# Kernel tuning notes

Hardware: AMD Instinct MI355X
Metric: run time of the kernel (lower is better)

Reference implementation:

```python
import jax, jax.numpy as jnp
import numpy as np

DIM = 256
NUM_RFS = 256
OUT_DIM = 1024
N = 65536
M = 0.001


def setup_inputs() -> dict:
    key = jax.random.key(0)
    k1, k2, k3, k4, k5, k6 = jax.random.split(key, 6)
    x = jax.random.normal(k1, (N, DIM), dtype=jnp.float32)
    input_weights = jax.random.normal(k2, (OUT_DIM, DIM), dtype=jnp.float32)
    b = jax.random.normal(k3, (OUT_DIM,), dtype=jnp.float32)
    # projection matrix: normal(mean=0, std=0.02, size=(num_rfs, dim))
    proj = 0.02 * jax.random.normal(k4, (NUM_RFS, DIM), dtype=jnp.float32)
    # xis are complex points of the random-feature construction; keep small for exp stability
    xis_real = 0.1 * jax.random.normal(k5, (NUM_RFS,), dtype=jnp.float32)
    xis_imag = 0.1 * jax.random.normal(k6, (NUM_RFS,), dtype=jnp.float32)
    return {"x": x, "input_weights": input_weights, "b": b, "proj": proj,
            "xis_real": xis_real, "xis_imag": xis_imag}


def _asym_feats(xw, xis, proj, bias, is_weight):
    """create_asym_feats with a_fun/b_fun = identity, A_fun/B_fun = exp(xi*b).
    xw: (rows, DIM) float; xis: (NUM_RFS,) complex64; proj: (NUM_RFS, DIM) float.
    Returns (rows, NUM_RFS) complex64."""
    ab = xis  # ab_fun is identity -> ab_coeffs = xis
    scale = np.sqrt(1.0 + 4.0 * M).astype(np.float32)
    # renorm_gs[i] = sqrt(1+4M) * ab[i] * gs[i]  -> (NUM_RFS, DIM) complex
    renorm_gs = scale * ab[:, None] * proj.astype(jnp.complex64)
    # dot_products = xw_c @ renorm_gs.T  -> (rows, NUM_RFS) complex
    dot = jnp.einsum('nd,rd->nr', xw.astype(jnp.complex64), renorm_gs)
    sq = jnp.sum(xw * xw, axis=-1)  # (rows,)
    # correction: outer(sq/2, ab*ab) + M*||g_i||^2 (broadcast over rows)
    corr = (sq[:, None] * 0.5) * (ab * ab)[None, :]
    corr = corr + M * jnp.sum(proj * proj, axis=-1)[None, :]
    feats = jnp.exp(dot - corr) * np.float32(1.0 / np.sqrt(NUM_RFS))
    if is_weight:
        # AB_coeffs[j, i] = exp(xis[i] * bias[j])
        AB = jnp.exp(xis[None, :] * bias[:, None].astype(jnp.complex64))
        feats = AB * feats
    return feats


def reference(x, input_weights, b, proj, xis_real, xis_imag):
    xis = (xis_real + 1j * xis_imag).astype(jnp.complex64)
    # normalize=False path: scale weights and bias by dim**-0.25 at init time
    inv4 = np.float32(1.0 / DIM ** 0.25)
    w = input_weights * inv4
    bb = b * inv4
    c = np.float32((1.0 / np.sqrt(2.0)) * (1.0 + 4.0 * M) ** (DIM / 4.0))
    # precomputed weight features (parameter of the module)
    w_plus = _asym_feats(w, xis, proj, bb, is_weight=True)
    w_minus = _asym_feats(w, -xis, proj, bb, is_weight=True)
    weights = c * jnp.concatenate([w_plus, w_minus], axis=-1)  # (OUT_DIM, 2R) complex
    # forward: x scaled by 1/dim (normalize=False)
    xs = x * np.float32(1.0 / DIM)
    f_plus = _asym_feats(xs, xis, proj, bb, is_weight=False)
    f_minus = _asym_feats(xs, -xis, proj, bb, is_weight=False)
    feat = c * jnp.concatenate([f_plus, f_minus], axis=-1)  # (N, 2R) complex
    # (feat @ weights.T).real
    out = jnp.einsum('nr,or->no', feat, weights).real
    return out
```

## Files before the change

### kernel.cpp

```cpp
#include <hip/hip_runtime.h>
#include <cmath>
#include <cstdint>

#define NROWS 65536
#define DIMN  256
#define NRF   256
#define OUTD  1024
#define KDIM  1024
#define MCOEF 0.001f

typedef __bf16 v8bf __attribute__((ext_vector_type(8)));
typedef float  v4f  __attribute__((ext_vector_type(4)));
typedef unsigned short us8 __attribute__((ext_vector_type(8)));

__device__ __forceinline__ unsigned short f2bf(float f) {
  unsigned int u = __float_as_uint(f);
  u += 0x7fffu + ((u >> 16) & 1u);
  return (unsigned short)(u >> 16);
}

__device__ __forceinline__ void async_copy16(const void* g, void* l) {
  __builtin_amdgcn_global_load_lds(
      (const __attribute__((address_space(1))) void*)g,
      (__attribute__((address_space(3))) void*)l, 16, 0, 0);
}

__device__ __forceinline__ int sw_slot(int r, int c) {
  return r * 4 + ((c ^ (r >> 1)) & 3);
}

__global__ __launch_bounds__(64) void prep_rf(
    const float* __restrict__ proj, unsigned short* __restrict__ projbf,
    float* __restrict__ mg2) {
  int i = blockIdx.x;
  int lane = threadIdx.x;
  float4 v = ((const float4*)(proj + (size_t)i * DIMN))[lane];
  ushort4 o;
  o.x = f2bf(v.x); o.y = f2bf(v.y); o.z = f2bf(v.z); o.w = f2bf(v.w);
  ((ushort4*)(projbf + (size_t)i * DIMN))[lane] = o;
  float ss = v.x * v.x + v.y * v.y + v.z * v.z + v.w * v.w;
#pragma unroll
  for (int off = 32; off > 0; off >>= 1) ss += __shfl_down(ss, off, 64);
  if (lane == 0) mg2[i] = MCOEF * ss;
}

__global__ __launch_bounds__(256) void fused_features(
    const float* __restrict__ src,
    float scl,
    const float* __restrict__ bias,
    float bscl,
    const float* __restrict__ xr_g, const float* __restrict__ xi_g,
    const float* __restrict__ mg2_g,
    const unsigned short* __restrict__ projbf,
    unsigned short* __restrict__ Fout,
    float sR, float sI, float scaleC) {
  __shared__ __align__(16) unsigned short big[16 * 1024];
  unsigned short* As = big;
  unsigned short* Bs = big + 2048;
  unsigned short* Os = big;
  __shared__ float xr_s[256], xi_s[256], c1_s[256], c2_s[256], mg2_s[256];
  __shared__ float sq_s[64], bias_s[64];

  int t = threadIdx.x;
  int lane = t & 63;
  int w = t >> 6;
  int blockRow = blockIdx.x * 64;

  {
    float a = xr_g[t], b = xi_g[t];
    xr_s[t] = a; xi_s[t] = b;
    c1_s[t] = a * a - b * b;
    c2_s[t] = 2.f * a * b;
    mg2_s[t] = mg2_g[t];
  }
  if (t < 64) bias_s[t] = bias ? bias[blockRow + t] * bscl : 0.f;

  v4f acc[4][4];
#pragma unroll
  for (int a = 0; a < 4; a++)
#pragma unroll
    for (int b = 0; b < 4; b++)
#pragma unroll
      for (int q = 0; q < 4; q++) acc[a][b][q] = 0.f;

  int arow = t >> 2, sub = t & 3;
  const float* srow = src + (size_t)(blockRow + arow) * DIMN + sub * 8;
  float ss = 0.f;

  for (int kb = 0; kb < DIMN; kb += 32) {
    float4 v0 = *(const float4*)(srow + kb);
    float4 v1 = *(const float4*)(srow + kb + 4);
    v0.x *= scl; v0.y *= scl; v0.z *= scl; v0.w *= scl;
    v1.x *= scl; v1.y *= scl; v1.z *= scl; v1.w *= scl;
    ss += v0.x * v0.x + v0.y * v0.y + v0.z * v0.z + v0.w * v0.w +
          v1.x * v1.x + v1.y * v1.y + v1.z * v1.z + v1.w * v1.w;
    us8 o;
    o[0] = f2bf(v0.x); o[1] = f2bf(v0.y); o[2] = f2bf(v0.z); o[3] = f2bf(v0.w);
    o[4] = f2bf(v1.x); o[5] = f2bf(v1.y); o[6] = f2bf(v1.z); o[7] = f2bf(v1.w);
    *(us8*)&As[sw_slot(arow, sub) * 8] = o;
#pragma unroll
    for (int r = 0; r < 4; r++) {
      int idx = r * 256 + t;
      int row = idx >> 2, kc = ((idx & 3) ^ ((idx >> 3) & 3)) * 8;
      async_copy16(projbf + (size_t)row * DIMN + kb + kc,
                   Bs + (idx & ~63) * 8);
    }
    __syncthreads();
    v8bf af[4], bfv[4];
    int c = lane >> 4;
#pragma unroll
    for (int mi = 0; mi < 4; mi++)
      af[mi] = *(const v8bf*)&As[sw_slot(mi * 16 + (lane & 15), c) * 8];
#pragma unroll
    for (int ni = 0; ni < 4; ni++)
      bfv[ni] = *(const v8bf*)&Bs[sw_slot(w * 64 + ni * 16 + (lane & 15), c) * 8];
#pragma unroll
    for (int mi = 0; mi < 4; mi++)
#pragma unroll
      for (int ni = 0; ni < 4; ni++)
        acc[mi][ni] = __builtin_amdgcn_mfma_f32_16x16x32_bf16(
            af[mi], bfv[ni], acc[mi][ni], 0, 0, 0);
    __syncthreads();
  }

  ss += __shfl_xor(ss, 1, 64);
  ss += __shfl_xor(ss, 2, 64);
  if (sub == 0) sq_s[arow] = ss;

#pragma unroll
  for (int mi = 0; mi < 4; mi++) {
    __syncthreads();
#pragma unroll
    for (int ni = 0; ni < 4; ni++) {
#pragma unroll
      for (int reg = 0; reg < 4; reg++) {
        int rl    = (lane >> 4) * 4 + reg;
        int rglob = mi * 16 + rl;
        int i     = w * 64 + ni * 16 + (lane & 15);
        float px = acc[mi][ni][reg];
        float tt = scaleC * px + bias_s[rglob];
        float u  = 0.5f * sq_s[rglob];
        float aa = u * c1_s[i] + mg2_s[i];
        float bb = u * c2_s[i];
        float txr = tt * xr_s[i];
        float txi = tt * xi_s[i];
        float erp = __expf(txr - aa);
        float erm = __expf(-txr - aa);
        float s1, cc1, s2, cc2;
        __sincosf(txi - bb, &s1, &cc1);
        __sincosf(txi + bb, &s2, &cc2);
        Os[rl * KDIM + i]            = f2bf(sR * erp * cc1);
        Os[rl * KDIM + NRF + i]      = f2bf(sR * erm * cc2);
        Os[rl * KDIM + 2 * NRF + i]  = f2bf(sI * erp * s1);
        Os[rl * KDIM + 3 * NRF + i]  = f2bf(-sI * erm * s2);
      }
    }
    __syncthreads();
#pragma unroll
    for (int j = 0; j < 8; j++) {
      int chunk = j * 256 + t;
      int rowo  = chunk >> 7;
      int off   = (chunk & 127) * 8;
      *(us8*)(Fout + (size_t)(blockRow + mi * 16 + rowo) * KDIM + off) =
          *(const us8*)&Os[rowo * KDIM + off];
    }
  }
}

__global__ __launch_bounds__(256) void gemm_bt(
    const unsigned short* __restrict__ A,
    const unsigned short* __restrict__ B,
    float* __restrict__ C) {
  __shared__ __align__(16) unsigned short As[128 * 32];
  __shared__ __align__(16) unsigned short Bs[128 * 32];
  int t = threadIdx.x;
  int lane = t & 63;
  int w = t >> 6;
  int wm = w >> 1, wn = w & 1;
  int lid = blockIdx.x;
  int slot = lid >> 3;
  size_t bm = (size_t)(((lid & 7) * 64) + (slot >> 3)) * 128;
  size_t bn = (size_t)(slot & 7) * 128;

  v4f acc[4][4];
#pragma unroll
  for (int a = 0; a < 4; a++)
#pragma unroll
    for (int b = 0; b < 4; b++)
#pragma unroll
      for (int q = 0; q < 4; q++) acc[a][b][q] = 0.f;

  for (int kb = 0; kb < KDIM; kb += 32) {
#pragma unroll
    for (int r = 0; r < 2; r++) {
      int idx = r * 256 + t;
      int row = idx >> 2, kc = ((idx & 3) ^ ((idx >> 3) & 3)) * 8;
      async_copy16(A + (bm + row) * KDIM + kb + kc, As + (idx & ~63) * 8);
      async_copy16(B + (bn + row) * KDIM + kb + kc, Bs + (idx & ~63) * 8);
    }
    __syncthreads();
    v8bf af[4], bfv[4];
    int c = lane >> 4;
#pragma unroll
    for (int mi = 0; mi < 4; mi++)
      af[mi] = *(const v8bf*)&As[sw_slot(wm * 64 + mi * 16 + (lane & 15), c) * 8];
#pragma unroll
    for (int ni = 0; ni < 4; ni++)
      bfv[ni] = *(const v8bf*)&Bs[sw_slot(wn * 64 + ni * 16 + (lane & 15), c) * 8];
#pragma unroll
    for (int mi = 0; mi < 4; mi++)
#pragma unroll
      for (int ni = 0; ni < 4; ni++)
        acc[mi][ni] = __builtin_amdgcn_mfma_f32_16x16x32_bf16(
            af[mi], bfv[ni], acc[mi][ni], 0, 0, 0);
    __syncthreads();
  }

#pragma unroll
  for (int mi = 0; mi < 4; mi++)
#pragma unroll
    for (int ni = 0; ni < 4; ni++)
#pragma unroll
      for (int reg = 0; reg < 4; reg++) {
        size_t row = bm + wm * 64 + mi * 16 + (lane >> 4) * 4 + reg;
        size_t col = bn + wn * 64 + ni * 16 + (lane & 15);
        C[row * OUTD + col] = acc[mi][ni][reg];
      }
}

extern "C" void kernel_launch(void* const* d_in, const int* in_sizes, int n_in,
                              void* d_out, int out_size, void* d_ws, size_t ws_size,
                              hipStream_t stream) {
  (void)in_sizes; (void)n_in; (void)out_size;
  const float* x    = (const float*)d_in[0];
  const float* iw   = (const float*)d_in[1];
  const float* bvec = (const float*)d_in[2];
  const float* proj = (const float*)d_in[3];
  const float* xr   = (const float*)d_in[4];
  const float* xi   = (const float*)d_in[5];
  float* out = (float*)d_out;

  char* ws = (char*)d_ws;
  size_t off = 0;
  auto take = [&](size_t bytes) {
    char* p = ws + off;
    off = (off + bytes + 255) & ~(size_t)255;
    return p;
  };
  unsigned short* F      = (unsigned short*)take((size_t)NROWS * KDIM * 2);
  unsigned short* Wp     = (unsigned short*)take((size_t)OUTD * KDIM * 2);
  unsigned short* projbf = (unsigned short*)take((size_t)NRF * DIMN * 2);
  float* mg2 = (float*)take((size_t)NRF * 4);
  if (ws_size < off) return;

  const float  scaleC = sqrtf(1.f + 4.f * MCOEF);
  const double c2d    = 0.5 * exp(128.0 * log(1.0 + 4.0 * 0.001));
  const float  invSR  = 0.0625f;
  const float  sRw    = (float)(c2d * 0.0625);

  prep_rf<<<NRF, 64, 0, stream>>>(proj, projbf, mg2);
  fused_features<<<NROWS / 64, 256, 0, stream>>>(
      x, 1.f / DIMN, nullptr, 0.f, xr, xi, mg2, projbf, F, invSR, invSR, scaleC);
  fused_features<<<OUTD / 64, 256, 0, stream>>>(
      iw, 0.25f, bvec, 0.25f, xr, xi, mg2, projbf, Wp, sRw, -sRw, scaleC);
  gemm_bt<<<4096, 256, 0, stream>>>(F, Wp, out);
}
```

Before: 567.4 us.

## Double-buffer GEMM LDS tiles, merge feature launches, interleave feature layout

The GEMM now stages the next K tile into a second LDS buffer with async copies while MFMAs run on the current tile, leaving one barrier per iteration. The two feature kernels are merged into a single launch that picks the weight or input path by block index. Feature outputs are written as interleaved 4-wide vectors (cos+, cos-, sin+, sin-) per random feature, changing the K ordering consistently for both operands so the stores become vectorized. Double buffering doubles LDS use per GEMM block, which may reduce occupancy.

After: 516.2 us. -9.0%, faster.

```diff
diff --git a/kernel.cpp b/kernel.cpp
--- a/kernel.cpp
+++ b/kernel.cpp
@@ -45,15 +45,15 @@
 }
 
 __global__ __launch_bounds__(256) void fused_features(
-    const float* __restrict__ src,
-    float scl,
-    const float* __restrict__ bias,
-    float bscl,
+    const float* __restrict__ srcX,
+    const float* __restrict__ srcW,
+    const float* __restrict__ biasW,
     const float* __restrict__ xr_g, const float* __restrict__ xi_g,
     const float* __restrict__ mg2_g,
     const unsigned short* __restrict__ projbf,
-    unsigned short* __restrict__ Fout,
-    float sR, float sI, float scaleC) {
+    unsigned short* __restrict__ FX,
+    unsigned short* __restrict__ FW,
+    float sRx, float sRw, float scaleC) {
   __shared__ __align__(16) unsigned short big[16 * 1024];
   unsigned short* As = big;
   unsigned short* Bs = big + 2048;
@@ -64,7 +64,14 @@
   int t = threadIdx.x;
   int lane = t & 63;
   int w = t >> 6;
-  int blockRow = blockIdx.x * 64;
+
+  bool isW = blockIdx.x < (OUTD / 64);
+  int blockRow = isW ? blockIdx.x * 64 : (blockIdx.x - OUTD / 64) * 64;
+  const float* src = isW ? srcW : srcX;
+  float scl = isW ? 0.25f : (1.f / DIMN);
+  unsigned short* Fout = isW ? FW : FX;
+  float sR = isW ? sRw : sRx;
+  float sI = isW ? -sRw : sRx;
 
   {
     float a = xr_g[t], b = xi_g[t];
@@ -73,7 +80,7 @@
     c2_s[t] = 2.f * a * b;
     mg2_s[t] = mg2_g[t];
   }
-  if (t < 64) bias_s[t] = bias ? bias[blockRow + t] * bscl : 0.f;
+  if (t < 64) bias_s[t] = isW ? biasW[blockRow + t] * 0.25f : 0.f;
 
   v4f acc[4][4];
 #pragma unroll
@@ -132,27 +139,31 @@
     __syncthreads();
 #pragma unroll
     for (int ni = 0; ni < 4; ni++) {
+      int i = w * 64 + ni * 16 + (lane & 15);
+      float xrv = xr_s[i], xiv = xi_s[i];
+      float c1v = c1_s[i], c2v = c2_s[i], mgv = mg2_s[i];
 #pragma unroll
       for (int reg = 0; reg < 4; reg++) {
         int rl    = (lane >> 4) * 4 + reg;
         int rglob = mi * 16 + rl;
-        int i     = w * 64 + ni * 16 + (lane & 15);
         float px = acc[mi][ni][reg];
         float tt = scaleC * px + bias_s[rglob];
         float u  = 0.5f * sq_s[rglob];
-        float aa = u * c1_s[i] + mg2_s[i];
-        float bb = u * c2_s[i];
-        float txr = tt * xr_s[i];
-        float txi = tt * xi_s[i];
+        float aa = u * c1v + mgv;
+        float bb = u * c2v;
+        float txr = tt * xrv;
+        float txi = tt * xiv;
         float erp = __expf(txr - aa);
         float erm = __expf(-txr - aa);
         float s1, cc1, s2, cc2;
         __sincosf(txi - bb, &s1, &cc1);
         __sincosf(txi + bb, &s2, &cc2);
-        Os[rl * KDIM + i]            = f2bf(sR * erp * cc1);
-        Os[rl * KDIM + NRF + i]      = f2bf(sR * erm * cc2);
-        Os[rl * KDIM + 2 * NRF + i]  = f2bf(sI * erp * s1);
-        Os[rl * KDIM + 3 * NRF + i]  = f2bf(-sI * erm * s2);
+        ushort4 ov;
+        ov.x = f2bf(sR * erp * cc1);
+        ov.y = f2bf(sR * erm * cc2);
+        ov.z = f2bf(sI * erp * s1);
+        ov.w = f2bf(-sI * erm * s2);
+        *(ushort4*)&Os[rl * KDIM + 4 * i] = ov;
       }
     }
     __syncthreads();
@@ -171,8 +182,8 @@
     const unsigned short* __restrict__ A,
     const unsigned short* __restrict__ B,
     float* __restrict__ C) {
-  __shared__ __align__(16) unsigned short As[128 * 32];
-  __shared__ __align__(16) unsigned short Bs[128 * 32];
+  __shared__ __align__(16) unsigned short As[2][128 * 32];
+  __shared__ __align__(16) unsigned short Bs[2][128 * 32];
   int t = threadIdx.x;
   int lane = t & 63;
   int w = t >> 6;
@@ -190,31 +201,45 @@
 #pragma unroll
       for (int q = 0; q < 4; q++) acc[a][b][q] = 0.f;
 
-  for (int kb = 0; kb < KDIM; kb += 32) {
+  auto stage = [&](int buf, int kb) {
 #pragma unroll
     for (int r = 0; r < 2; r++) {
       int idx = r * 256 + t;
       int row = idx >> 2, kc = ((idx & 3) ^ ((idx >> 3) & 3)) * 8;
-      async_copy16(A + (bm + row) * KDIM + kb + kc, As + (idx & ~63) * 8);
-      async_copy16(B + (bn + row) * KDIM + kb + kc, Bs + (idx & ~63) * 8);
-    }
-    __syncthreads();
+      async_copy16(A + (bm + row) * KDIM + kb + kc, &As[buf][(idx & ~63) * 8]);
+      async_copy16(B + (bn + row) * KDIM + kb + kc, &Bs[buf][(idx & ~63) * 8]);
+    }
+  };
+
+  auto compute_tile = [&](int buf) {
     v8bf af[4], bfv[4];
     int c = lane >> 4;
 #pragma unroll
     for (int mi = 0; mi < 4; mi++)
-      af[mi] = *(const v8bf*)&As[sw_slot(wm * 64 + mi * 16 + (lane & 15), c) * 8];
+      af[mi] = *(const v8bf*)&As[buf][sw_slot(wm * 64 + mi * 16 + (lane & 15), c) * 8];
 #pragma unroll
     for (int ni = 0; ni < 4; ni++)
-      bfv[ni] = *(const v8bf*)&Bs[sw_slot(wn * 64 + ni * 16 + (lane & 15), c) * 8];
+      bfv[ni] = *(const v8bf*)&Bs[buf][sw_slot(wn * 64 + ni * 16 + (lane & 15), c) * 8];
 #pragma unroll
     for (int mi = 0; mi < 4; mi++)
 #pragma unroll
       for (int ni = 0; ni < 4; ni++)
         acc[mi][ni] = __builtin_amdgcn_mfma_f32_16x16x32_bf16(
             af[mi], bfv[ni], acc[mi][ni], 0, 0, 0);
-    __syncthreads();
-  }
+  };
+
+  stage(0, 0);
+  asm volatile("s_waitcnt vmcnt(0)" ::: "memory");
+  __syncthreads();
+  int cur = 0;
+  for (int kb = 32; kb < KDIM; kb += 32) {
+    stage(cur ^ 1, kb);
+    compute_tile(cur);
+    asm volatile("s_waitcnt vmcnt(0)" ::: "memory");
+    __syncthreads();
+    cur ^= 1;
+  }
+  compute_tile(cur);
 
 #pragma unroll
   for (int mi = 0; mi < 4; mi++)
@@ -259,9 +284,7 @@
   const float  sRw    = (float)(c2d * 0.0625);
 
   prep_rf<<<NRF, 64, 0, stream>>>(proj, projbf, mg2);
-  fused_features<<<NROWS / 64, 256, 0, stream>>>(
-      x, 1.f / DIMN, nullptr, 0.f, xr, xi, mg2, projbf, F, invSR, invSR, scaleC);
-  fused_features<<<OUTD / 64, 256, 0, stream>>>(
-      iw, 0.25f, bvec, 0.25f, xr, xi, mg2, projbf, Wp, sRw, -sRw, scaleC);
+  fused_features<<<NROWS / 64 + OUTD / 64, 256, 0, stream>>>(
+      x, iw, bvec, xr, xi, mg2, projbf, F, Wp, invSR, sRw, scaleC);
   gemm_bt<<<4096, 256, 0, stream>>>(F, Wp, out);
 }
```
